# Kernel optimization log

Hardware: AMD Instinct MI355X
Metric: run time of the kernel (lower is better)

The kernel has to match this reference:

```python
import jax, jax.numpy as jnp
import numpy as np

N = 2_000_000   # num_nodes
C = 128         # in_channels
B = 256         # num graphs
K = 32          # max branches per graph (branch ids in [0, K))
NEG_SLOPE = 0.01  # torch leaky_relu default


def setup_inputs() -> dict:
    key = jax.random.key(0)
    k1, k2, k3, k4, k5, k6 = jax.random.split(key, 6)
    node_embed = jax.random.normal(k1, (N, C), dtype=jnp.float32)
    batch = jnp.sort(jax.random.randint(k2, (N,), 0, B, dtype=jnp.int64))
    branch = jax.random.randint(k3, (N,), 0, K, dtype=jnp.int64)
    s1 = 1.0 / np.sqrt(C)
    W1 = jax.random.uniform(k4, (C, C), jnp.float32, -s1, s1)
    b1 = jnp.zeros((C,), jnp.float32)
    W2 = jax.random.uniform(k5, (C, 1), jnp.float32, -s1, s1)
    b2 = jnp.zeros((1,), jnp.float32)
    return {"node_embed": node_embed, "batch": batch, "branch": branch,
            "W1": W1, "b1": b1, "W2": W2, "b2": b2}


def reference(node_embed, batch, branch, W1, b1, W2, b2):
    # Original code compacts branch ids via per-graph offsets (cumsum of max+1).
    # Equivalent static-shape formulation: global slot id = batch*K + branch,
    # and a per-graph mask keeping slots b <= max(branch in graph) — exactly the
    # branches 0..num_branch_per_graph-1 that repeat_interleave covers (including
    # empty branches below the max, whose pooled embed is 0 -> MLP(0)).
    gid = batch * K + branch                               # [N]
    branch_embed = jax.ops.segment_sum(node_embed, gid, num_segments=B * K)  # [B*K, C]
    h = branch_embed @ W1 + b1
    h = jnp.where(h >= 0, h, NEG_SLOPE * h)                # leaky_relu
    branch_value = h @ W2 + b2                             # [B*K, 1]
    max_b = jax.ops.segment_max(branch, batch, num_segments=B)  # [B]
    mask = (jnp.arange(K)[None, :] <= max_b[:, None]).astype(branch_value.dtype)  # [B, K]
    graph_value = jnp.sum(branch_value.reshape(B, K) * mask, axis=1, keepdims=True)  # [B, 1]
    return graph_value
```

## Files before the change

### kernel.cpp

```cpp
#include <hip/hip_runtime.h>

#define NCH 128
#define NGR 256
#define NBR 32
#define NEG_SLOPE 0.01f

typedef __attribute__((ext_vector_type(8))) short bf16x8;
typedef __attribute__((ext_vector_type(4))) float f32x4;

constexpr int TROWS = 64;

__device__ inline unsigned short rtne_bf16(float x) {
    unsigned u = __float_as_uint(x);
    return (unsigned short)((u + 0x7FFFu + ((u >> 16) & 1u)) >> 16);
}

template <bool TAIL>
__device__ inline void compute_tile(
    const float (*__restrict__ buf)[NCH], const int* __restrict__ sbr, int rem,
    int c, int gq, int m,
    f32x4& acc0, f32x4& acc1, int& mymax)
{
    #pragma unroll
    for (int kk = 0; kk < 2; ++kk) {
        const int rb = kk * 32 + gq * 8;
        int idv[8];
        {
            const int4 i0 = *(const int4*)&sbr[rb];
            const int4 i1 = *(const int4*)&sbr[rb + 4];
            idv[0] = i0.x; idv[1] = i0.y; idv[2] = i0.z; idv[3] = i0.w;
            idv[4] = i1.x; idv[5] = i1.y; idv[6] = i1.z; idv[7] = i1.w;
        }
        bf16x8 a0, a1, bhi, blo;
        #pragma unroll
        for (int j = 0; j < 8; ++j) {
            const float v = buf[rb + j][c * 16 + m];
            const unsigned u = __float_as_uint(v);
            const unsigned short h = (unsigned short)(u >> 16);
            const float hf = __uint_as_float(u & 0xFFFF0000u);
            const unsigned short l = rtne_bf16(v - hf);
            bhi[j] = (short)h;
            blo[j] = (short)l;
            bool val = true;
            if (TAIL) val = (rb + j) < rem;
            a0[j] = (val && idv[j] == m)      ? (short)0x3F80 : (short)0;
            a1[j] = (val && idv[j] == m + 16) ? (short)0x3F80 : (short)0;
            if (val) mymax = max(mymax, idv[j]);
        }
        acc0 = __builtin_amdgcn_mfma_f32_16x16x32_bf16(a0, bhi, acc0, 0, 0, 0);
        acc0 = __builtin_amdgcn_mfma_f32_16x16x32_bf16(a0, blo, acc0, 0, 0, 0);
        acc1 = __builtin_amdgcn_mfma_f32_16x16x32_bf16(a1, bhi, acc1, 0, 0, 0);
        acc1 = __builtin_amdgcn_mfma_f32_16x16x32_bf16(a1, blo, acc1, 0, 0, 0);
    }
}

__global__ __launch_bounds__(512, 4) void scatter_mfma(
    const float* __restrict__ node_embed,
    const int*   __restrict__ batch,
    const int*   __restrict__ branch,
    float*       __restrict__ part,
    int*         __restrict__ max_b_part,
    int n_nodes)
{
    __shared__ float buf[2][TROWS][NCH] __attribute__((aligned(16)));
    __shared__ int   sbr_i[2][TROWS]    __attribute__((aligned(16)));
    __shared__ int   seg_s[2];
    __shared__ int   wm[8];

    const int t    = threadIdx.x;
    const int bid  = blockIdx.x;
    const int g    = bid >> 1;
    const int half = bid & 1;
    const int wave = t >> 6;
    const int lane = t & 63;
    const int c    = wave;
    const int gq   = lane >> 4;
    const int m    = lane & 15;

    if (t < 2) {
        const int target = g + t;
        int lo = 0, hi = n_nodes;
        while (lo < hi) { int mid = (lo + hi) >> 1; if (batch[mid] < target) lo = mid + 1; else hi = mid; }
        seg_s[t] = lo;
    }
    __syncthreads();
    const int s0 = seg_s[0], s1 = seg_s[1];
    const int nt_tot = (s1 - s0 + TROWS - 1) / TROWS;
    const int ntA    = (nt_tot + 1) >> 1;
    const int sa     = half ? s0 + ntA * TROWS : s0;
    const int nt     = half ? nt_tot - ntA : ntA;

    auto stage = [&](int ti2) {
        const int c0n = sa + ti2 * TROWS;
        const int nb  = ti2 & 1;
        #pragma unroll
        for (int u = 0; u < 4; ++u) {
            const int koff = (u * 8 + wave) * 1024;
            const size_t lanebyte = (size_t)koff + (size_t)lane * 16;
            const int rowg = c0n + (int)(lanebyte >> 9);
            const char* src = (const char*)node_embed + (((size_t)c0n << 9) + lanebyte);
            if (rowg >= s1)
                src = (const char*)node_embed;
            __builtin_amdgcn_global_load_lds(
                (const __attribute__((address_space(1))) void*)src,
                (__attribute__((address_space(3))) void*)((char*)&buf[nb][0][0] + koff),
                16, 0, 0);
        }
        if (wave == 0) {
            const int i0 = min(c0n + lane, n_nodes - 1);
            __builtin_amdgcn_global_load_lds(
                (const __attribute__((address_space(1))) void*)(branch + i0),
                (__attribute__((address_space(3))) void*)((char*)&sbr_i[nb][0]), 4, 0, 0);
        }
    };

    f32x4 acc0 = {0.f, 0.f, 0.f, 0.f};
    f32x4 acc1 = {0.f, 0.f, 0.f, 0.f};
    int mymax = -1;

    if (nt > 0) {
        stage(0);
        if (nt > 1) stage(1);
        if (nt > 1) {
            if (wave == 0) asm volatile("s_waitcnt vmcnt(5)" ::: "memory");
            else           asm volatile("s_waitcnt vmcnt(4)" ::: "memory");
        } else {
            asm volatile("s_waitcnt vmcnt(0)" ::: "memory");
        }
        __builtin_amdgcn_s_barrier();
        __builtin_amdgcn_sched_barrier(0);

        for (int ti = 0; ti < nt; ++ti) {
            const int cb = ti & 1;
            if (ti == nt - 1)
                compute_tile<true >(buf[cb], sbr_i[cb], s1 - (sa + ti * TROWS),
                                    c, gq, m, acc0, acc1, mymax);
            else
                compute_tile<false>(buf[cb], sbr_i[cb], 0,
                                    c, gq, m, acc0, acc1, mymax);

            __builtin_amdgcn_s_barrier();
            __builtin_amdgcn_sched_barrier(0);

            const bool more = (ti + 2 < nt);
            if (more) stage(ti + 2);
            if (ti + 1 < nt) {
                if (more) {
                    if (wave == 0) asm volatile("s_waitcnt vmcnt(5)" ::: "memory");
                    else           asm volatile("s_waitcnt vmcnt(4)" ::: "memory");
                } else {
                    asm volatile("s_waitcnt vmcnt(0)" ::: "memory");
                }
                __builtin_amdgcn_s_barrier();
                __builtin_amdgcn_sched_barrier(0);
            }
        }
    }

    {
        const int sr = gq * 4;
        float* be = part + (size_t)half * NGR * NBR * NCH
                  + (size_t)g * NBR * NCH + (size_t)c * 16 + m;
        #pragma unroll
        for (int r = 0; r < 4; ++r) {
            be[(sr + r) * NCH]      = acc0[r];
            be[(16 + sr + r) * NCH] = acc1[r];
        }
    }

    int v = mymax;
    #pragma unroll
    for (int off = 32; off > 0; off >>= 1) v = max(v, __shfl_down(v, off));
    if (lane == 0) wm[wave] = v;
    __syncthreads();
    if (t == 0) {
        int mb = wm[0];
        #pragma unroll
        for (int i = 1; i < 8; ++i) mb = max(mb, wm[i]);
        max_b_part[half * NGR + g] = mb;
    }
}

__global__ __launch_bounds__(256) void mlp_kernel(
    const float* __restrict__ part,
    const int*   __restrict__ max_b_part,
    const float* __restrict__ W1,
    const float* __restrict__ b1,
    const float* __restrict__ W2,
    const float* __restrict__ b2,
    float*       __restrict__ out)
{
    __shared__ float W1s[NCH * NCH];
    __shared__ float b1s[NCH], W2s[NCH];
    __shared__ float rows[2][NCH];
    __shared__ float red[2][NCH];
    __shared__ float sval[NBR];

    const int t = threadIdx.x;
    const int b = blockIdx.x;

    for (int i = t; i < NCH * NCH / 4; i += 256)
        ((float4*)W1s)[i] = ((const float4*)W1)[i];
    if (t < NCH) { b1s[t] = b1[t]; W2s[t] = W2[t]; }
    __syncthreads();

    const int half = t >> 7;
    const int j    = t & 127;
    const float* p1 = part + (size_t)NGR * NBR * NCH;

    for (int k0 = 0; k0 < NBR; k0 += 2) {
        const int slot = k0 + half;
        const size_t idx = ((size_t)b * NBR + slot) * NCH + j;
        rows[half][j] = part[idx] + p1[idx];
        __syncthreads();

        float h = b1s[j];
        #pragma unroll 8
        for (int i = 0; i < NCH; ++i)
            h += rows[half][i] * W1s[i * NCH + j];
        h = (h >= 0.0f) ? h : NEG_SLOPE * h;
        red[half][j] = h * W2s[j];
        __syncthreads();

        for (int off = 64; off > 0; off >>= 1) {
            if (j < off) red[half][j] += red[half][j + off];
            __syncthreads();
        }
        if (j == 0) sval[slot] = red[half][0];
        __syncthreads();
    }

    if (t < 64) {
        const int mb = max(max_b_part[b], max_b_part[NGR + b]);
        float v = (t < NBR && t <= mb) ? (sval[t] + b2[0]) : 0.0f;
        #pragma unroll
        for (int off = 32; off > 0; off >>= 1) v += __shfl_down(v, off);
        if (t == 0) out[b] = v;
    }
}

extern "C" void kernel_launch(void* const* d_in, const int* in_sizes, int n_in,
                              void* d_out, int out_size, void* d_ws, size_t ws_size,
                              hipStream_t stream) {
    const float* node_embed = (const float*)d_in[0];
    const int*   batch      = (const int*)d_in[1];
    const int*   branch     = (const int*)d_in[2];
    const float* W1         = (const float*)d_in[3];
    const float* b1         = (const float*)d_in[4];
    const float* W2         = (const float*)d_in[5];
    const float* b2         = (const float*)d_in[6];
    float*       out        = (float*)d_out;

    const int n_nodes = in_sizes[0] / NCH;

    float* part = (float*)d_ws;
    int*   max_b_part = (int*)((char*)d_ws + 2 * (size_t)NGR * NBR * NCH * sizeof(float));

    scatter_mfma<<<2 * NGR, 512, 0, stream>>>(node_embed, batch, branch,
                                              part, max_b_part, n_nodes);
    mlp_kernel<<<NGR, 256, 0, stream>>>(part, max_b_part, W1, b1, W2, b2, out);
}
```

Baseline: 233.2 us.

## Replace LDS double-buffer staging with direct register loads and shuffled branch ids

Drops the shared-memory double buffer fed by global_load_lds, along with its barriers. Each lane now loads its own column values straight into registers, with software prefetch of the next tile into a second register set. Branch ids are fetched once per lane and broadcast with __shfl instead of being read from LDS. This removes LDS traffic and block-wide synchronisation, but the global loads become strided 4-byte accesses rather than 16-byte coalesced ones, and register pressure and shuffle count go up.

After: 263.0 us. +12.8%, slower.

```diff
diff --git a/kernel.cpp b/kernel.cpp
--- a/kernel.cpp
+++ b/kernel.cpp
@@ -13,45 +13,6 @@
 __device__ inline unsigned short rtne_bf16(float x) {
     unsigned u = __float_as_uint(x);
     return (unsigned short)((u + 0x7FFFu + ((u >> 16) & 1u)) >> 16);
-}
-
-template <bool TAIL>
-__device__ inline void compute_tile(
-    const float (*__restrict__ buf)[NCH], const int* __restrict__ sbr, int rem,
-    int c, int gq, int m,
-    f32x4& acc0, f32x4& acc1, int& mymax)
-{
-    #pragma unroll
-    for (int kk = 0; kk < 2; ++kk) {
-        const int rb = kk * 32 + gq * 8;
-        int idv[8];
-        {
-            const int4 i0 = *(const int4*)&sbr[rb];
-            const int4 i1 = *(const int4*)&sbr[rb + 4];
-            idv[0] = i0.x; idv[1] = i0.y; idv[2] = i0.z; idv[3] = i0.w;
-            idv[4] = i1.x; idv[5] = i1.y; idv[6] = i1.z; idv[7] = i1.w;
-        }
-        bf16x8 a0, a1, bhi, blo;
-        #pragma unroll
-        for (int j = 0; j < 8; ++j) {
-            const float v = buf[rb + j][c * 16 + m];
-            const unsigned u = __float_as_uint(v);
-            const unsigned short h = (unsigned short)(u >> 16);
-            const float hf = __uint_as_float(u & 0xFFFF0000u);
-            const unsigned short l = rtne_bf16(v - hf);
-            bhi[j] = (short)h;
-            blo[j] = (short)l;
-            bool val = true;
-            if (TAIL) val = (rb + j) < rem;
-            a0[j] = (val && idv[j] == m)      ? (short)0x3F80 : (short)0;
-            a1[j] = (val && idv[j] == m + 16) ? (short)0x3F80 : (short)0;
-            if (val) mymax = max(mymax, idv[j]);
-        }
-        acc0 = __builtin_amdgcn_mfma_f32_16x16x32_bf16(a0, bhi, acc0, 0, 0, 0);
-        acc0 = __builtin_amdgcn_mfma_f32_16x16x32_bf16(a0, blo, acc0, 0, 0, 0);
-        acc1 = __builtin_amdgcn_mfma_f32_16x16x32_bf16(a1, bhi, acc1, 0, 0, 0);
-        acc1 = __builtin_amdgcn_mfma_f32_16x16x32_bf16(a1, blo, acc1, 0, 0, 0);
-    }
 }
 
 __global__ __launch_bounds__(512, 4) void scatter_mfma(
@@ -62,10 +23,8 @@
     int*         __restrict__ max_b_part,
     int n_nodes)
 {
-    __shared__ float buf[2][TROWS][NCH] __attribute__((aligned(16)));
-    __shared__ int   sbr_i[2][TROWS]    __attribute__((aligned(16)));
-    __shared__ int   seg_s[2];
-    __shared__ int   wm[8];
+    __shared__ int seg_s[2];
+    __shared__ int wm[8];
 
     const int t    = threadIdx.x;
     const int bid  = blockIdx.x;
@@ -90,70 +49,66 @@
     const int sa     = half ? s0 + ntA * TROWS : s0;
     const int nt     = half ? nt_tot - ntA : ntA;
 
-    auto stage = [&](int ti2) {
-        const int c0n = sa + ti2 * TROWS;
-        const int nb  = ti2 & 1;
-        #pragma unroll
-        for (int u = 0; u < 4; ++u) {
-            const int koff = (u * 8 + wave) * 1024;
-            const size_t lanebyte = (size_t)koff + (size_t)lane * 16;
-            const int rowg = c0n + (int)(lanebyte >> 9);
-            const char* src = (const char*)node_embed + (((size_t)c0n << 9) + lanebyte);
-            if (rowg >= s1)
-                src = (const char*)node_embed;
-            __builtin_amdgcn_global_load_lds(
-                (const __attribute__((address_space(1))) void*)src,
-                (__attribute__((address_space(3))) void*)((char*)&buf[nb][0][0] + koff),
-                16, 0, 0);
-        }
-        if (wave == 0) {
-            const int i0 = min(c0n + lane, n_nodes - 1);
-            __builtin_amdgcn_global_load_lds(
-                (const __attribute__((address_space(1))) void*)(branch + i0),
-                (__attribute__((address_space(3))) void*)((char*)&sbr_i[nb][0]), 4, 0, 0);
-        }
-    };
+    const float* colp = node_embed + (size_t)(c * 16 + m);
+    const int last = (s1 > 0) ? (s1 - 1) : 0;
 
     f32x4 acc0 = {0.f, 0.f, 0.f, 0.f};
     f32x4 acc1 = {0.f, 0.f, 0.f, 0.f};
     int mymax = -1;
 
+    auto issue = [&](int ti, float* d, int& vid) {
+        const int rb = sa + ti * TROWS;
+        #pragma unroll
+        for (int kk = 0; kk < 2; ++kk)
+            #pragma unroll
+            for (int j = 0; j < 8; ++j) {
+                int row = rb + kk * 32 + gq * 8 + j;
+                row = min(row, last);
+                d[kk * 8 + j] = colp[(size_t)row * NCH];
+            }
+        vid = branch[min(rb + lane, n_nodes - 1)];
+    };
+
+    auto compute = [&](int ti, const float* d, int vid) {
+        const int rb  = sa + ti * TROWS;
+        const int rem = s1 - rb;
+        if (rb + lane < s1) mymax = max(mymax, vid);
+        #pragma unroll
+        for (int kk = 0; kk < 2; ++kk) {
+            bf16x8 a0, a1, bhi, blo;
+            #pragma unroll
+            for (int j = 0; j < 8; ++j) {
+                const float v = d[kk * 8 + j];
+                const unsigned u = __float_as_uint(v);
+                const unsigned short h = (unsigned short)(u >> 16);
+                const float hf = __uint_as_float(u & 0xFFFF0000u);
+                const unsigned short l = rtne_bf16(v - hf);
+                bhi[j] = (short)h;
+                blo[j] = (short)l;
+                const int idj = __shfl(vid, kk * 32 + gq * 8 + j);
+                const bool val = (kk * 32 + gq * 8 + j) < rem;
+                a0[j] = (val && idj == m)      ? (short)0x3F80 : (short)0;
+                a1[j] = (val && idj == m + 16) ? (short)0x3F80 : (short)0;
+            }
+            acc0 = __builtin_amdgcn_mfma_f32_16x16x32_bf16(a0, bhi, acc0, 0, 0, 0);
+            acc0 = __builtin_amdgcn_mfma_f32_16x16x32_bf16(a0, blo, acc0, 0, 0, 0);
+            acc1 = __builtin_amdgcn_mfma_f32_16x16x32_bf16(a1, bhi, acc1, 0, 0, 0);
+            acc1 = __builtin_amdgcn_mfma_f32_16x16x32_bf16(a1, blo, acc1, 0, 0, 0);
+        }
+    };
+
     if (nt > 0) {
-        stage(0);
-        if (nt > 1) stage(1);
-        if (nt > 1) {
-            if (wave == 0) asm volatile("s_waitcnt vmcnt(5)" ::: "memory");
-            else           asm volatile("s_waitcnt vmcnt(4)" ::: "memory");
-        } else {
-            asm volatile("s_waitcnt vmcnt(0)" ::: "memory");
-        }
-        __builtin_amdgcn_s_barrier();
-        __builtin_amdgcn_sched_barrier(0);
-
-        for (int ti = 0; ti < nt; ++ti) {
-            const int cb = ti & 1;
-            if (ti == nt - 1)
-                compute_tile<true >(buf[cb], sbr_i[cb], s1 - (sa + ti * TROWS),
-                                    c, gq, m, acc0, acc1, mymax);
-            else
-                compute_tile<false>(buf[cb], sbr_i[cb], 0,
-                                    c, gq, m, acc0, acc1, mymax);
-
-            __builtin_amdgcn_s_barrier();
-            __builtin_amdgcn_sched_barrier(0);
-
-            const bool more = (ti + 2 < nt);
-            if (more) stage(ti + 2);
-            if (ti + 1 < nt) {
-                if (more) {
-                    if (wave == 0) asm volatile("s_waitcnt vmcnt(5)" ::: "memory");
-                    else           asm volatile("s_waitcnt vmcnt(4)" ::: "memory");
-                } else {
-                    asm volatile("s_waitcnt vmcnt(0)" ::: "memory");
-                }
-                __builtin_amdgcn_s_barrier();
-                __builtin_amdgcn_sched_barrier(0);
-            }
+        float dA[16], dB[16];
+        int vA, vB;
+        issue(0, dA, vA);
+        int ti = 0;
+        for (;;) {
+            if (ti + 1 < nt) issue(ti + 1, dB, vB);
+            compute(ti, dA, vA);
+            if (++ti >= nt) break;
+            if (ti + 1 < nt) issue(ti + 1, dA, vA);
+            compute(ti, dB, vB);
+            if (++ti >= nt) break;
         }
     }
 
```

## Rewrite MLP stage with split-bf16 MFMA and triple-buffer scatter pipeline

Applied to the files above, without the earlier changes.

The MLP kernel's scalar FP32 dot-product loop and its barrier-heavy tree reductions are replaced by a 512-thread MFMA version. It packs W1 and the pooled branch embeddings into hi/lo bf16 pairs and uses three MFMAs per step to approximate FP32 accuracy. The scatter kernel moves from a 64-row double buffer to a 32-row triple buffer, issuing prefetch two tiles ahead before waiting on the current tile. The goal is to cut the serial MLP latency and keep more loads in flight, at the cost of more barriers per row processed and a small precision change from dropping the lo*lo term.

Result: faster. 210.0 us (-9.9%).

```diff
diff --git a/kernel.cpp b/kernel.cpp
--- a/kernel.cpp
+++ b/kernel.cpp
@@ -8,50 +8,18 @@
 typedef __attribute__((ext_vector_type(8))) short bf16x8;
 typedef __attribute__((ext_vector_type(4))) float f32x4;
 
-constexpr int TROWS = 64;
+constexpr int TROWS = 32;
 
 __device__ inline unsigned short rtne_bf16(float x) {
     unsigned u = __float_as_uint(x);
     return (unsigned short)((u + 0x7FFFu + ((u >> 16) & 1u)) >> 16);
 }
-
-template <bool TAIL>
-__device__ inline void compute_tile(
-    const float (*__restrict__ buf)[NCH], const int* __restrict__ sbr, int rem,
-    int c, int gq, int m,
-    f32x4& acc0, f32x4& acc1, int& mymax)
-{
-    #pragma unroll
-    for (int kk = 0; kk < 2; ++kk) {
-        const int rb = kk * 32 + gq * 8;
-        int idv[8];
-        {
-            const int4 i0 = *(const int4*)&sbr[rb];
-            const int4 i1 = *(const int4*)&sbr[rb + 4];
-            idv[0] = i0.x; idv[1] = i0.y; idv[2] = i0.z; idv[3] = i0.w;
-            idv[4] = i1.x; idv[5] = i1.y; idv[6] = i1.z; idv[7] = i1.w;
-        }
-        bf16x8 a0, a1, bhi, blo;
-        #pragma unroll
-        for (int j = 0; j < 8; ++j) {
-            const float v = buf[rb + j][c * 16 + m];
-            const unsigned u = __float_as_uint(v);
-            const unsigned short h = (unsigned short)(u >> 16);
-            const float hf = __uint_as_float(u & 0xFFFF0000u);
-            const unsigned short l = rtne_bf16(v - hf);
-            bhi[j] = (short)h;
-            blo[j] = (short)l;
-            bool val = true;
-            if (TAIL) val = (rb + j) < rem;
-            a0[j] = (val && idv[j] == m)      ? (short)0x3F80 : (short)0;
-            a1[j] = (val && idv[j] == m + 16) ? (short)0x3F80 : (short)0;
-            if (val) mymax = max(mymax, idv[j]);
-        }
-        acc0 = __builtin_amdgcn_mfma_f32_16x16x32_bf16(a0, bhi, acc0, 0, 0, 0);
-        acc0 = __builtin_amdgcn_mfma_f32_16x16x32_bf16(a0, blo, acc0, 0, 0, 0);
-        acc1 = __builtin_amdgcn_mfma_f32_16x16x32_bf16(a1, bhi, acc1, 0, 0, 0);
-        acc1 = __builtin_amdgcn_mfma_f32_16x16x32_bf16(a1, blo, acc1, 0, 0, 0);
-    }
+__device__ inline unsigned pack_hl(float v) {
+    const unsigned u = __float_as_uint(v);
+    const unsigned short h = (unsigned short)(u >> 16);
+    const float hf = __uint_as_float(u & 0xFFFF0000u);
+    const unsigned short l = rtne_bf16(v - hf);
+    return ((unsigned)h << 16) | (unsigned)l;
 }
 
 __global__ __launch_bounds__(512, 4) void scatter_mfma(
@@ -62,8 +30,8 @@
     int*         __restrict__ max_b_part,
     int n_nodes)
 {
-    __shared__ float buf[2][TROWS][NCH] __attribute__((aligned(16)));
-    __shared__ int   sbr_i[2][TROWS]    __attribute__((aligned(16)));
+    __shared__ float buf[3][TROWS][NCH] __attribute__((aligned(16)));
+    __shared__ int   sbr_i[3][64]       __attribute__((aligned(16)));
     __shared__ int   seg_s[2];
     __shared__ int   wm[8];
 
@@ -90,27 +58,25 @@
     const int sa     = half ? s0 + ntA * TROWS : s0;
     const int nt     = half ? nt_tot - ntA : ntA;
 
-    auto stage = [&](int ti2) {
-        const int c0n = sa + ti2 * TROWS;
-        const int nb  = ti2 & 1;
-        #pragma unroll
-        for (int u = 0; u < 4; ++u) {
+    auto stage = [&](int ti, int bi) {
+        const int c0n = sa + ti * TROWS;
+        #pragma unroll
+        for (int u = 0; u < 2; ++u) {
             const int koff = (u * 8 + wave) * 1024;
-            const size_t lanebyte = (size_t)koff + (size_t)lane * 16;
-            const int rowg = c0n + (int)(lanebyte >> 9);
-            const char* src = (const char*)node_embed + (((size_t)c0n << 9) + lanebyte);
-            if (rowg >= s1)
-                src = (const char*)node_embed;
+            const int lanebyte = koff + lane * 16;
+            const int rowg = c0n + (lanebyte >> 9);
+            const char* src = (const char*)node_embed + ((size_t)c0n * 512 + (size_t)lanebyte);
+            if (rowg >= s1) src = (const char*)node_embed;
             __builtin_amdgcn_global_load_lds(
                 (const __attribute__((address_space(1))) void*)src,
-                (__attribute__((address_space(3))) void*)((char*)&buf[nb][0][0] + koff),
+                (__attribute__((address_space(3))) void*)((char*)&buf[bi][0][0] + koff),
                 16, 0, 0);
         }
         if (wave == 0) {
             const int i0 = min(c0n + lane, n_nodes - 1);
             __builtin_amdgcn_global_load_lds(
                 (const __attribute__((address_space(1))) void*)(branch + i0),
-                (__attribute__((address_space(3))) void*)((char*)&sbr_i[nb][0]), 4, 0, 0);
+                (__attribute__((address_space(3))) void*)((char*)&sbr_i[bi][0]), 4, 0, 0);
         }
     };
 
@@ -118,12 +84,36 @@
     f32x4 acc1 = {0.f, 0.f, 0.f, 0.f};
     int mymax = -1;
 
+    auto compute = [&](int ti, int bi) {
+        const int rem = s1 - (sa + ti * TROWS);
+        const int4 i0 = *(const int4*)&sbr_i[bi][gq * 8];
+        const int4 i1 = *(const int4*)&sbr_i[bi][gq * 8 + 4];
+        const int idv[8] = {i0.x, i0.y, i0.z, i0.w, i1.x, i1.y, i1.z, i1.w};
+        bf16x8 a0, a1, bh, bl;
+        #pragma unroll
+        for (int j = 0; j < 8; ++j) {
+            const float v = buf[bi][gq * 8 + j][c * 16 + m];
+            const unsigned u = __float_as_uint(v);
+            bh[j] = (short)(unsigned short)(u >> 16);
+            const float hf = __uint_as_float(u & 0xFFFF0000u);
+            bl[j] = (short)rtne_bf16(v - hf);
+            const bool val = (gq * 8 + j) < rem;
+            a0[j] = (val && idv[j] == m)      ? (short)0x3F80 : (short)0;
+            a1[j] = (val && idv[j] == m + 16) ? (short)0x3F80 : (short)0;
+            if (val) mymax = max(mymax, idv[j]);
+        }
+        acc0 = __builtin_amdgcn_mfma_f32_16x16x32_bf16(a0, bh, acc0, 0, 0, 0);
+        acc0 = __builtin_amdgcn_mfma_f32_16x16x32_bf16(a0, bl, acc0, 0, 0, 0);
+        acc1 = __builtin_amdgcn_mfma_f32_16x16x32_bf16(a1, bh, acc1, 0, 0, 0);
+        acc1 = __builtin_amdgcn_mfma_f32_16x16x32_bf16(a1, bl, acc1, 0, 0, 0);
+    };
+
     if (nt > 0) {
-        stage(0);
-        if (nt > 1) stage(1);
+        stage(0, 0);
+        if (nt > 1) stage(1, 1);
         if (nt > 1) {
-            if (wave == 0) asm volatile("s_waitcnt vmcnt(5)" ::: "memory");
-            else           asm volatile("s_waitcnt vmcnt(4)" ::: "memory");
+            if (wave == 0) asm volatile("s_waitcnt vmcnt(3)" ::: "memory");
+            else           asm volatile("s_waitcnt vmcnt(2)" ::: "memory");
         } else {
             asm volatile("s_waitcnt vmcnt(0)" ::: "memory");
         }
@@ -131,29 +121,23 @@
         __builtin_amdgcn_sched_barrier(0);
 
         for (int ti = 0; ti < nt; ++ti) {
-            const int cb = ti & 1;
-            if (ti == nt - 1)
-                compute_tile<true >(buf[cb], sbr_i[cb], s1 - (sa + ti * TROWS),
-                                    c, gq, m, acc0, acc1, mymax);
-            else
-                compute_tile<false>(buf[cb], sbr_i[cb], 0,
-                                    c, gq, m, acc0, acc1, mymax);
-
+            const int bi = ti % 3;
+            if (ti + 2 < nt) stage(ti + 2, (ti + 2) % 3);
+            const int k = min(nt - 1 - ti, 2);
+            if (wave == 0) {
+                if (k == 2)      asm volatile("s_waitcnt vmcnt(6)" ::: "memory");
+                else if (k == 1) asm volatile("s_waitcnt vmcnt(3)" ::: "memory");
+                else             asm volatile("s_waitcnt vmcnt(0)" ::: "memory");
+            } else {
+                if (k == 2)      asm volatile("s_waitcnt vmcnt(4)" ::: "memory");
+                else if (k == 1) asm volatile("s_waitcnt vmcnt(2)" ::: "memory");
+                else             asm volatile("s_waitcnt vmcnt(0)" ::: "memory");
+            }
             __builtin_amdgcn_s_barrier();
             __builtin_amdgcn_sched_barrier(0);
-
-            const bool more = (ti + 2 < nt);
-            if (more) stage(ti + 2);
-            if (ti + 1 < nt) {
-                if (more) {
-                    if (wave == 0) asm volatile("s_waitcnt vmcnt(5)" ::: "memory");
-                    else           asm volatile("s_waitcnt vmcnt(4)" ::: "memory");
-                } else {
-                    asm volatile("s_waitcnt vmcnt(0)" ::: "memory");
-                }
-                __builtin_amdgcn_s_barrier();
-                __builtin_amdgcn_sched_barrier(0);
-            }
+            compute(ti, bi);
+            __builtin_amdgcn_s_barrier();
+            __builtin_amdgcn_sched_barrier(0);
         }
     }
 
@@ -181,7 +165,7 @@
     }
 }
 
-__global__ __launch_bounds__(256) void mlp_kernel(
+__global__ __launch_bounds__(512) void mlp_mfma(
     const float* __restrict__ part,
     const int*   __restrict__ max_b_part,
     const float* __restrict__ W1,
@@ -190,52 +174,110 @@
     const float* __restrict__ b2,
     float*       __restrict__ out)
 {
-    __shared__ float W1s[NCH * NCH];
-    __shared__ float b1s[NCH], W2s[NCH];
-    __shared__ float rows[2][NCH];
-    __shared__ float red[2][NCH];
-    __shared__ float sval[NBR];
-
-    const int t = threadIdx.x;
-    const int b = blockIdx.x;
-
-    for (int i = t; i < NCH * NCH / 4; i += 256)
-        ((float4*)W1s)[i] = ((const float4*)W1)[i];
-    if (t < NCH) { b1s[t] = b1[t]; W2s[t] = W2[t]; }
+    __shared__ unsigned w1p[128 * 130];
+    __shared__ unsigned epk[32 * 132];
+    __shared__ float    red[32 * 8];
+
+    const int t    = threadIdx.x;
+    const int g    = blockIdx.x;
+    const int wave = t >> 6;
+    const int lane = t & 63;
+    const int gq   = lane >> 4;
+    const int m    = lane & 15;
+    const int sh   = wave & 1;
+    const int c0   = wave >> 1;
+
+    #pragma unroll
+    for (int i = 0; i < 8; ++i) {
+        const int eb  = i * 2048 + t * 4;
+        const int row = eb >> 7, col = eb & 127;
+        const float4 w = *(const float4*)&W1[eb];
+        unsigned* d = &w1p[row * 130 + col];
+        *(uint2*)d       = make_uint2(pack_hl(w.x), pack_hl(w.y));
+        *(uint2*)(d + 2) = make_uint2(pack_hl(w.z), pack_hl(w.w));
+    }
+    {
+        const int slot = t >> 4, kb = (t & 15) * 8;
+        const size_t base = ((size_t)g * NBR + slot) * NCH + kb;
+        const float* pB = part + (size_t)NGR * NBR * NCH;
+        float4 e0 = *(const float4*)&part[base];
+        float4 e1 = *(const float4*)&part[base + 4];
+        const float4 f0 = *(const float4*)&pB[base];
+        const float4 f1 = *(const float4*)&pB[base + 4];
+        e0.x += f0.x; e0.y += f0.y; e0.z += f0.z; e0.w += f0.w;
+        e1.x += f1.x; e1.y += f1.y; e1.z += f1.z; e1.w += f1.w;
+        unsigned* d = &epk[slot * 132 + kb];
+        *(uint4*)d       = make_uint4(pack_hl(e0.x), pack_hl(e0.y), pack_hl(e0.z), pack_hl(e0.w));
+        *(uint4*)(d + 4) = make_uint4(pack_hl(e1.x), pack_hl(e1.y), pack_hl(e1.z), pack_hl(e1.w));
+    }
+    const float b1v0 = b1[c0 * 16 + m],      b1v1 = b1[(c0 + 4) * 16 + m];
+    const float w2v0 = W2[c0 * 16 + m],      w2v1 = W2[(c0 + 4) * 16 + m];
     __syncthreads();
 
-    const int half = t >> 7;
-    const int j    = t & 127;
-    const float* p1 = part + (size_t)NGR * NBR * NCH;
-
-    for (int k0 = 0; k0 < NBR; k0 += 2) {
-        const int slot = k0 + half;
-        const size_t idx = ((size_t)b * NBR + slot) * NCH + j;
-        rows[half][j] = part[idx] + p1[idx];
-        __syncthreads();
-
-        float h = b1s[j];
-        #pragma unroll 8
-        for (int i = 0; i < NCH; ++i)
-            h += rows[half][i] * W1s[i * NCH + j];
-        h = (h >= 0.0f) ? h : NEG_SLOPE * h;
-        red[half][j] = h * W2s[j];
-        __syncthreads();
-
-        for (int off = 64; off > 0; off >>= 1) {
-            if (j < off) red[half][j] += red[half][j + off];
-            __syncthreads();
-        }
-        if (j == 0) sval[slot] = red[half][0];
-        __syncthreads();
-    }
+    f32x4 accA = {0.f, 0.f, 0.f, 0.f};
+    f32x4 accB = {0.f, 0.f, 0.f, 0.f};
+    #pragma unroll
+    for (int ks = 0; ks < 4; ++ks) {
+        const int k0 = ks * 32;
+        const unsigned* ap = &epk[(sh * 16 + m) * 132 + k0 + gq * 8];
+        const uint4 aw0 = *(const uint4*)ap;
+        const uint4 aw1 = *(const uint4*)(ap + 4);
+        const unsigned aw[8] = {aw0.x, aw0.y, aw0.z, aw0.w, aw1.x, aw1.y, aw1.z, aw1.w};
+        bf16x8 ah, al;
+        #pragma unroll
+        for (int j = 0; j < 8; ++j) { ah[j] = (short)(aw[j] >> 16); al[j] = (short)(aw[j] & 0xFFFFu); }
+
+        bf16x8 bh, blo;
+        #pragma unroll
+        for (int j = 0; j < 8; ++j) {
+            const unsigned w = w1p[(k0 + gq * 8 + j) * 130 + c0 * 16 + m];
+            bh[j] = (short)(w >> 16); blo[j] = (short)(w & 0xFFFFu);
+        }
+        accA = __builtin_amdgcn_mfma_f32_16x16x32_bf16(ah, bh,  accA, 0, 0, 0);
+        accA = __builtin_amdgcn_mfma_f32_16x16x32_bf16(al, bh,  accA, 0, 0, 0);
+        accA = __builtin_amdgcn_mfma_f32_16x16x32_bf16(ah, blo, accA, 0, 0, 0);
+
+        #pragma unroll
+        for (int j = 0; j < 8; ++j) {
+            const unsigned w = w1p[(k0 + gq * 8 + j) * 130 + (c0 + 4) * 16 + m];
+            bh[j] = (short)(w >> 16); blo[j] = (short)(w & 0xFFFFu);
+        }
+        accB = __builtin_amdgcn_mfma_f32_16x16x32_bf16(ah, bh,  accB, 0, 0, 0);
+        accB = __builtin_amdgcn_mfma_f32_16x16x32_bf16(al, bh,  accB, 0, 0, 0);
+        accB = __builtin_amdgcn_mfma_f32_16x16x32_bf16(ah, blo, accB, 0, 0, 0);
+    }
+
+    #pragma unroll
+    for (int r = 0; r < 4; ++r) {
+        float h0 = accA[r] + b1v0;
+        h0 = (h0 >= 0.f) ? h0 : NEG_SLOPE * h0;
+        float s0v = h0 * w2v0;
+        float h1 = accB[r] + b1v1;
+        h1 = (h1 >= 0.f) ? h1 : NEG_SLOPE * h1;
+        float s1v = h1 * w2v1;
+        #pragma unroll
+        for (int off = 1; off < 16; off <<= 1) {
+            s0v += __shfl_xor(s0v, off);
+            s1v += __shfl_xor(s1v, off);
+        }
+        if (m == 0) {
+            const int slot = sh * 16 + gq * 4 + r;
+            red[slot * 8 + c0]     = s0v;
+            red[slot * 8 + c0 + 4] = s1v;
+        }
+    }
+    __syncthreads();
 
     if (t < 64) {
-        const int mb = max(max_b_part[b], max_b_part[NGR + b]);
-        float v = (t < NBR && t <= mb) ? (sval[t] + b2[0]) : 0.0f;
-        #pragma unroll
-        for (int off = 32; off > 0; off >>= 1) v += __shfl_down(v, off);
-        if (t == 0) out[b] = v;
+        const int rr = lane & 31;
+        float v = 0.f;
+        #pragma unroll
+        for (int cc = 0; cc < 8; ++cc) v += red[rr * 8 + cc];
+        const int mb = max(max_b_part[g], max_b_part[NGR + g]);
+        float val = (lane < 32 && rr <= mb) ? (v + b2[0]) : 0.f;
+        #pragma unroll
+        for (int off = 32; off > 0; off >>= 1) val += __shfl_down(val, off);
+        if (t == 0) out[g] = val;
     }
 }
 
@@ -258,5 +300,5 @@
 
     scatter_mfma<<<2 * NGR, 512, 0, stream>>>(node_embed, batch, branch,
                                               part, max_b_part, n_nodes);
-    mlp_kernel<<<NGR, 256, 0, stream>>>(part, max_b_part, W1, b1, W2, b2, out);
-}
+    mlp_mfma<<<NGR, 512, 0, stream>>>(part, max_b_part, W1, b1, W2, b2, out);
+}
```
